# Performance work log

Hardware: AMD Instinct MI355X
Metric: run time of the kernel (lower is better)

The kernel has to match this reference:

```python
import jax, jax.numpy as jnp
import numpy as np

N_NODES = 100000
N_EDGES = 1600000
HIDDEN = 128
STEPS = 4
N_GRAPHS = 64


def setup_inputs() -> dict:
    key = jax.random.key(0)
    ks = jax.random.split(key, 8)
    x = jax.random.normal(ks[0], (N_NODES, HIDDEN), dtype=jnp.float32)
    edge_index = jax.random.randint(ks[1], (2, N_EDGES), 0, N_NODES, dtype=jnp.int64)
    batch = jnp.sort(jax.random.randint(ks[2], (N_NODES,), 0, N_GRAPHS, dtype=jnp.int64))
    s = 1.0 / np.sqrt(HIDDEN)
    weight = jax.random.normal(ks[3], (STEPS, HIDDEN, HIDDEN), dtype=jnp.float32) * s
    w_ih = jax.random.normal(ks[4], (3 * HIDDEN, HIDDEN), dtype=jnp.float32) * s
    w_hh = jax.random.normal(ks[5], (3 * HIDDEN, HIDDEN), dtype=jnp.float32) * s
    b_ih = jnp.zeros((3 * HIDDEN,), dtype=jnp.float32)
    b_hh = jnp.zeros((3 * HIDDEN,), dtype=jnp.float32)
    return {"x": x, "edge_index": edge_index, "batch": batch,
            "weight": weight, "w_ih": w_ih, "w_hh": w_hh,
            "b_ih": b_ih, "b_hh": b_hh}


def _gru_cell(m, h, w_ih, w_hh, b_ih, b_hh):
    # PyTorch GRUCell: gates ordered (r, z, n)
    gi = m @ w_ih.T + b_ih  # [N, 3H]
    gh = h @ w_hh.T + b_hh  # [N, 3H]
    i_r, i_z, i_n = jnp.split(gi, 3, axis=-1)
    h_r, h_z, h_n = jnp.split(gh, 3, axis=-1)
    r = jax.nn.sigmoid(i_r + h_r)
    z = jax.nn.sigmoid(i_z + h_z)
    n = jnp.tanh(i_n + r * h_n)
    return (1.0 - z) * n + z * h


def reference(x, edge_index, batch, weight, w_ih, w_hh, b_ih, b_hh):
    src, dst = edge_index[0], edge_index[1]
    h = x
    for i in range(STEPS):
        m = h @ weight[i]  # [N, H]
        # message = m[src] scattered (add) into dst
        aggr = jax.ops.segment_sum(m[src], dst, num_segments=N_NODES)
        h = _gru_cell(aggr, h, w_ih, w_hh, b_ih, b_hh)
    h = jax.nn.relu(h)
    # global mean pool per graph
    sums = jax.ops.segment_sum(h, batch, num_segments=N_GRAPHS)  # [G, H]
    counts = jax.ops.segment_sum(jnp.ones((N_NODES,), h.dtype), batch, num_segments=N_GRAPHS)
    return sums / jnp.maximum(counts, 1.0)[:, None]
```

## Files before the change

kernel.cpp:

```cpp
#include <hip/hip_runtime.h>

#define N_NODES  100000
#define N_EDGES  1600000
#define HIDDEN   128
#define STEPS    4
#define N_GRAPHS 64
#define NBUCK    256
#define BWID     391
#define BCAP     7168

typedef unsigned short u16;
typedef unsigned int   u32;
typedef unsigned long long u64;
typedef __attribute__((ext_vector_type(8))) short bf16x8;
typedef __attribute__((ext_vector_type(4))) float f32x4;
typedef __attribute__((ext_vector_type(2))) float f32x2;

__device__ inline u16 f2bf(float f) {
  u32 u = __float_as_uint(f);
  u = (u + 0x7FFFu + ((u >> 16) & 1u)) >> 16;
  return (u16)u;
}
__device__ inline float bf2f(u16 b) { return __uint_as_float(((u32)b) << 16); }

__device__ inline float rcp_f(float x) { return __builtin_amdgcn_rcpf(x); }
__device__ inline float sig_f(float x) { return rcp_f(1.f + __expf(-x)); }
__device__ inline float tanh_f(float x) { return 1.f - 2.f * rcp_f(1.f + __expf(2.f * x)); }

__global__ __launch_bounds__(1024) void k_part(const int* __restrict__ esrc,
                                               const int* __restrict__ edst,
                                               int* __restrict__ gcursor,
                                               u32* __restrict__ ebuf) {
  __shared__ int hist[16][NBUCK];
  __shared__ int base[16][NBUCK];
  int tid = threadIdx.x;
  int wv  = tid >> 6;
  #pragma unroll
  for (int i = 0; i < 4; ++i) ((int*)hist)[tid + i * 1024] = 0;
  __syncthreads();
  int e0 = blockIdx.x * 4096;
  int sv[4], dv[4], bk[4], rk[4];
  #pragma unroll
  for (int i = 0; i < 4; ++i) {
    int e = e0 + i * 1024 + tid;
    if (e < N_EDGES) {
      sv[i] = esrc[e];
      dv[i] = edst[e];
      bk[i] = (int)((u32)dv[i] / (u32)BWID);
      rk[i] = atomicAdd(&hist[wv][bk[i]], 1);
    } else bk[i] = -1;
  }
  __syncthreads();
  if (tid < NBUCK) {
    int c[16];
    int sum = 0;
    #pragma unroll
    for (int w = 0; w < 16; ++w) { c[w] = hist[w][tid]; sum += c[w]; }
    int g = atomicAdd(&gcursor[tid], sum);
    #pragma unroll
    for (int w = 0; w < 16; ++w) { base[w][tid] = g; g += c[w]; }
  }
  __syncthreads();
  #pragma unroll
  for (int i = 0; i < 4; ++i) {
    if (bk[i] >= 0) {
      int pos = bk[i] * BCAP + base[wv][bk[i]] + rk[i];
      ebuf[pos] = ((u32)(dv[i] - bk[i] * BWID) << 17) | (u32)sv[i];
    }
  }
}

__global__ void k_bscan(const int* __restrict__ gcursor, int* __restrict__ ebase,
                        float* __restrict__ acc) {
  __shared__ int buf[NBUCK];
  int t = threadIdx.x;
  int v = gcursor[t];
  buf[t] = v;
  __syncthreads();
  for (int off = 1; off < NBUCK; off <<= 1) {
    int u = 0;
    if (t >= off) u = buf[t - off];
    __syncthreads();
    buf[t] += u;
    __syncthreads();
  }
  ebase[t] = buf[t] - v;
  if (t == NBUCK - 1) ebase[NBUCK] = buf[t];
  for (int i = t; i < N_GRAPHS * HIDDEN; i += NBUCK) acc[i] = 0.f;
}

__global__ __launch_bounds__(1024) void k_csr(const u32* __restrict__ ebuf,
                                              const int* __restrict__ ebase,
                                              int* __restrict__ offs,
                                              int* __restrict__ csr) {
  __shared__ int lcnt[512];
  __shared__ int lofs[512];
  int b = blockIdx.x, tid = threadIdx.x;
  int n0 = b * BWID;
  int n1 = min(n0 + BWID, N_NODES);
  int nn = n1 - n0;
  int e0 = ebase[b];
  int cnt = ebase[b + 1] - e0;
  const u32* ebase_p = ebuf + (size_t)b * BCAP;
  if (tid < 512) lcnt[tid] = 0;
  __syncthreads();
  for (int e = tid; e < cnt; e += 1024) {
    int dst = (int)(ebase_p[e] >> 17);
    atomicAdd(&lcnt[dst], 1);
  }
  __syncthreads();
  if (tid < 512) lofs[tid] = lcnt[tid];
  __syncthreads();
  for (int off = 1; off < 512; off <<= 1) {
    int v = 0;
    if (tid < 512 && tid >= off) v = lofs[tid - off];
    __syncthreads();
    if (tid < 512 && tid >= off) lofs[tid] += v;
    __syncthreads();
  }
  int nodeoff = 0;
  if (tid < 512) nodeoff = e0 + lofs[tid] - lcnt[tid];
  if (tid < 512) lofs[tid] = nodeoff;
  if (tid < nn) offs[n0 + tid] = nodeoff;
  if (b == 0 && tid == 0) offs[N_NODES] = N_EDGES;
  __syncthreads();
  for (int e = tid; e < cnt; e += 1024) {
    u32 p = ebase_p[e];
    int src = (int)(p & 0x1FFFFu);
    int dst = (int)(p >> 17);
    int pos = atomicAdd(&lofs[dst], 1);
    csr[pos] = src;
  }
}

__global__ void k_wb(const float* __restrict__ W, const float* __restrict__ w_ih,
                     const float* __restrict__ w_hh, u16* __restrict__ bsw) {
  __shared__ float wrow[128];
  int b = blockIdx.x, st = b >> 8, k = b & 255, t = threadIdx.x;
  if (k < 128) wrow[t] = W[(st * 128 + k) * 128 + t];
  __syncthreads();
  int kc = k >> 5, quad = (k >> 3) & 3, kl = k & 7;
  u16* base = bsw + (size_t)st * 131072 + kc * 16384;
  #pragma unroll
  for (int gq = 0; gq < 4; ++gq) {
    int c = gq * 128 + t;
    float v;
    if (k < 128) {
      if (c < 384) {
        const float* wr = w_ih + c * 128;
        float sacc = 0.f;
        for (int j = 0; j < 128; ++j) sacc += wrow[j] * wr[j];
        v = sacc;
      } else v = 0.f;
    } else {
      int kk = k - 128;
      if (c < 256)      v = w_hh[c * 128 + kk];
      else if (c < 384) v = 0.f;
      else              v = w_hh[(c - 128) * 128 + kk];
    }
    int gi = c >> 7, cw = c & 127;
    int wv = cw >> 5, hu = (cw >> 4) & 1, nl = c & 15;
    int slot = wv * 8 + gi * 2 + hu;
    base[(slot * 4 + quad) * 128 + nl * 8 + kl] = f2bf(v);
  }
}

__global__ void k_convert(const float* __restrict__ x, u16* __restrict__ h0,
                          u16* __restrict__ h1) {
  int i = (blockIdx.x * 256 + threadIdx.x) * 4;
  float4 v = *(const float4*)(x + i);
  u16 o[4] = {f2bf(v.x), f2bf(v.y), f2bf(v.z), f2bf(v.w)};
  *(uint2*)(h0 + i) = *(uint2*)o;
  if (blockIdx.x == 0) {
    int t = threadIdx.x;
    if (t < 64)       ((u32*)(h0 + (size_t)N_NODES * 128))[t] = 0;
    else if (t < 128) ((u32*)(h1 + (size_t)N_NODES * 128))[t - 64] = 0;
  }
}

__device__ inline void acc8(f32x2* a, uint4 p) {
  f32x2 v;
  v.x = __uint_as_float(p.x << 16); v.y = __uint_as_float(p.x & 0xffff0000u);
  a[0] += v;
  v.x = __uint_as_float(p.y << 16); v.y = __uint_as_float(p.y & 0xffff0000u);
  a[1] += v;
  v.x = __uint_as_float(p.z << 16); v.y = __uint_as_float(p.z & 0xffff0000u);
  a[2] += v;
  v.x = __uint_as_float(p.w << 16); v.y = __uint_as_float(p.w & 0xffff0000u);
  a[3] += v;
}
__device__ inline uint4 ldrow(const char* hb, u32 off) {
  return *(const uint4*)(hb + off);
}

__global__ __launch_bounds__(256, 2) void k_fused(
    const u16* __restrict__ h_mat, const int* __restrict__ csr,
    const int* __restrict__ offs, const u16* __restrict__ bsw,
    const float* __restrict__ b_ih, const float* __restrict__ b_hh,
    u16* __restrict__ h_out) {
  __shared__ u16 Asw[8192];

  const int tid  = threadIdx.x;
  const int wave = tid >> 6;
  const int lane = tid & 63;
  const int nl   = lane & 15;
  const int quad = lane >> 4;
  const int row0 = blockIdx.x * 32;

  {
    int snl = tid & 15, squad = (tid >> 4) & 3, sel = tid >> 6;
    if (sel >= 2) {
      int g = sel & 1;
      const u16* row = h_mat + (size_t)(row0 + g * 16 + snl) * 128;
      #pragma unroll
      for (int kc2 = 0; kc2 < 4; ++kc2) {
        uint4 v = *(const uint4*)(row + kc2 * 32 + squad * 8);
        *(uint4*)&Asw[(((g * 8 + 4 + kc2) * 4 + squad) * 16 + snl) * 8] = v;
      }
    }
  }

  {
    const char* hb = (const char*)h_mat;
    const int q   = lane >> 4;
    const int sub = lane & 15;
    const u32 co  = (u32)(sub * 16);
    #pragma unroll 1
    for (int i = 0; i < 8; ++i) {
      int n    = wave * 8 + i;
      int node = row0 + n;
      int beg = offs[node], end = offs[node + 1];
      f32x2 a[4];
      a[0] = a[1] = a[2] = a[3] = (f32x2){0.f, 0.f};
      int j = beg + q;
      for (; j + 12 < end; j += 16) {
        u32 s0 = (u32)csr[j], s1 = (u32)csr[j + 4], s2 = (u32)csr[j + 8], s3 = (u32)csr[j + 12];
        uint4 p0 = ldrow(hb, (s0 << 8) | co);
        uint4 p1 = ldrow(hb, (s1 << 8) | co);
        uint4 p2 = ldrow(hb, (s2 << 8) | co);
        uint4 p3 = ldrow(hb, (s3 << 8) | co);
        acc8(a, p0); acc8(a, p1); acc8(a, p2); acc8(a, p3);
      }
      {
        int j0 = j, j1 = j + 4, j2 = j + 8, j3 = j + 12;
        int t0 = (j0 < end) ? j0 : 0, t1 = (j1 < end) ? j1 : 0;
        int t2 = (j2 < end) ? j2 : 0, t3 = (j3 < end) ? j3 : 0;
        u32 s0 = (u32)csr[t0]; s0 = (j0 < end) ? s0 : (u32)N_NODES;
        u32 s1 = (u32)csr[t1]; s1 = (j1 < end) ? s1 : (u32)N_NODES;
        u32 s2 = (u32)csr[t2]; s2 = (j2 < end) ? s2 : (u32)N_NODES;
        u32 s3 = (u32)csr[t3]; s3 = (j3 < end) ? s3 : (u32)N_NODES;
        uint4 p0 = ldrow(hb, (s0 << 8) | co);
        uint4 p1 = ldrow(hb, (s1 << 8) | co);
        uint4 p2 = ldrow(hb, (s2 << 8) | co);
        uint4 p3 = ldrow(hb, (s3 << 8) | co);
        acc8(a, p0); acc8(a, p1); acc8(a, p2); acc8(a, p3);
      }
      #pragma unroll
      for (int r = 0; r < 4; ++r) {
        a[r].x += __shfl_xor(a[r].x, 16); a[r].x += __shfl_xor(a[r].x, 32);
        a[r].y += __shfl_xor(a[r].y, 16); a[r].y += __shfl_xor(a[r].y, 32);
      }
      if (q == 0) {
        uint4 o;
        o.x = (u32)f2bf(a[0].x) | ((u32)f2bf(a[0].y) << 16);
        o.y = (u32)f2bf(a[1].x) | ((u32)f2bf(a[1].y) << 16);
        o.z = (u32)f2bf(a[2].x) | ((u32)f2bf(a[2].y) << 16);
        o.w = (u32)f2bf(a[3].x) | ((u32)f2bf(a[3].y) << 16);
        int g = n >> 4, snl = n & 15;
        *(uint4*)&Asw[(((g * 8 + (sub >> 2)) * 4 + (sub & 3)) * 16 + snl) * 8] = o;
      }
    }
  }
  __syncthreads();

  const u16* bp = bsw + wave * 8 * 512 + lane * 8;

  f32x4 acc[2][8];
  #pragma unroll
  for (int g = 0; g < 2; ++g)
    #pragma unroll
    for (int u = 0; u < 8; ++u) acc[g][u] = (f32x4){0.f, 0.f, 0.f, 0.f};

  bf16x8 b0[6], b1[6], b2[6];
  #pragma unroll
  for (int i = 0; i < 6; ++i) b0[i] = *(const bf16x8*)(bp + i * 512);
  #pragma unroll
  for (int i = 0; i < 6; ++i) b1[i] = *(const bf16x8*)(bp + 16384 + i * 512);

  #pragma unroll
  for (int kc = 0; kc < 8; ++kc) {
    if (kc < 6) {
      #pragma unroll
      for (int i = 0; i < 6; ++i) {
        int us = (kc + 2 < 4) ? i : (i < 4 ? i : i + 2);
        b2[i] = *(const bf16x8*)(bp + (kc + 2) * 16384 + us * 512);
      }
    }
    bf16x8 a0 = *(const bf16x8*)&Asw[kc * 512 + lane * 8];
    bf16x8 a1 = *(const bf16x8*)&Asw[(8 + kc) * 512 + lane * 8];
    #pragma unroll
    for (int i = 0; i < 6; ++i) {
      int u = (kc < 4) ? i : (i < 4 ? i : i + 2);
      acc[0][u] = __builtin_amdgcn_mfma_f32_16x16x32_bf16(a0, b0[i], acc[0][u], 0, 0, 0);
      acc[1][u] = __builtin_amdgcn_mfma_f32_16x16x32_bf16(a1, b0[i], acc[1][u], 0, 0, 0);
    }
    #pragma unroll
    for (int i = 0; i < 6; ++i) { b0[i] = b1[i]; b1[i] = b2[i]; }
  }

  float bias[8];
  #pragma unroll
  for (int u = 0; u < 8; ++u) {
    int gi = u >> 1, hu = u & 1;
    int cw = wave * 32 + hu * 16 + nl;
    bias[u] = (gi == 0) ? b_ih[cw] + b_hh[cw]
            : (gi == 1) ? b_ih[128 + cw] + b_hh[128 + cw]
            : (gi == 2) ? b_ih[256 + cw]
                        : b_hh[256 + cw];
  }

  #pragma unroll
  for (int g = 0; g < 2; ++g) {
    #pragma unroll
    for (int hu = 0; hu < 2; ++hu) {
      int cw = wave * 32 + hu * 16 + nl;
      int hbase = ((g * 8 + 4 + wave) * 4 + ((hu * 2 + (nl >> 3)) & 3)) * 128 + (nl & 7);
      #pragma unroll
      for (int i = 0; i < 4; ++i) {
        int m = quad * 4 + i;
        float rv = sig_f(acc[g][0 + hu][i] + bias[0 + hu]);
        float zv = sig_f(acc[g][2 + hu][i] + bias[2 + hu]);
        float iv = acc[g][4 + hu][i] + bias[4 + hu];
        float hn = acc[g][6 + hu][i] + bias[6 + hu];
        float hv = bf2f(Asw[hbase + m * 8]);
        float n  = tanh_f(iv + rv * hn);
        float o  = n + zv * (hv - n);
        h_out[(size_t)(row0 + g * 16 + m) * 128 + cw] = f2bf(o);
      }
    }
  }
}

__global__ void k_pool_partial(const u16* __restrict__ h, const int* __restrict__ batch,
                               float* __restrict__ acc) {
  int t = threadIdx.x;
  int node0 = blockIdx.x * 125;
  int node1 = node0 + 125;
  int cur = batch[node0];
  float sum = 0.f;
  for (int r = node0; r < node1; ++r) {
    int g = batch[r];
    if (g != cur) {
      atomicAdd(&acc[cur * 128 + t], sum);
      sum = 0.f;
      cur = g;
    }
    sum += fmaxf(bf2f(h[(size_t)r * 128 + t]), 0.f);
  }
  atomicAdd(&acc[cur * 128 + t], sum);
}

__global__ void k_pool_div(const float* __restrict__ acc, const int* __restrict__ batch,
                           float* __restrict__ out) {
  __shared__ int se[2];
  int g = blockIdx.x, t = threadIdx.x;
  if (t < 2) {
    int target = g + t;
    int lo = 0, hi = N_NODES;
    while (lo < hi) { int mid = (lo + hi) >> 1; if (batch[mid] < target) lo = mid + 1; else hi = mid; }
    se[t] = lo;
  }
  __syncthreads();
  int cnt = se[1] - se[0];
  out[g * 128 + t] = acc[g * 128 + t] / (float)(cnt > 0 ? cnt : 1);
}

extern "C" void kernel_launch(void* const* d_in, const int* in_sizes, int n_in,
                              void* d_out, int out_size, void* d_ws, size_t ws_size,
                              hipStream_t stream) {
  const float* x     = (const float*)d_in[0];
  const int*   edges = (const int*)d_in[1];
  const int*   batch = (const int*)d_in[2];
  const float* W     = (const float*)d_in[3];
  const float* w_ih  = (const float*)d_in[4];
  const float* w_hh  = (const float*)d_in[5];
  const float* b_ih  = (const float*)d_in[6];
  const float* b_hh  = (const float*)d_in[7];
  float* out = (float*)d_out;

  char* w = (char*)d_ws;
  u16* buf0    = (u16*)(w);
  u16* buf1    = (u16*)(w + 25600256);
  u16* bsw     = (u16*)(w + 51200512);
  float* acc   = (float*)(w + 52249088);
  int* offs    = (int*)(w + 52281856);
  int* gcursor = (int*)(w + 52682240);
  int* ebase   = (int*)(w + 52683264);
  int* csr     = (int*)(w + 52684800);
  u32* ebuf    = (u32*)buf1;

  const int* esrc = edges;
  const int* edst = edges + N_EDGES;

  hipMemsetAsync(gcursor, 0, NBUCK * sizeof(int), stream);
  k_part<<<391, 1024, 0, stream>>>(esrc, edst, gcursor, ebuf);
  k_bscan<<<1, NBUCK, 0, stream>>>(gcursor, ebase, acc);
  k_csr<<<NBUCK, 1024, 0, stream>>>(ebuf, ebase, offs, csr);
  k_wb<<<1024, 128, 0, stream>>>(W, w_ih, w_hh, bsw);
  k_convert<<<(N_NODES * HIDDEN) / 1024, 256, 0, stream>>>(x, buf0, buf1);

  u16* hcur = buf0;
  u16* hnxt = buf1;
  for (int st = 0; st < STEPS; ++st) {
    k_fused<<<N_NODES / 32, 256, 0, stream>>>(hcur, csr, offs, bsw + st * 131072,
                                              b_ih, b_hh, hnxt);
    u16* tmp = hcur; hcur = hnxt; hnxt = tmp;
  }
  k_pool_partial<<<800, 128, 0, stream>>>(hcur, batch, acc);
  k_pool_div<<<N_GRAPHS, 128, 0, stream>>>(acc, batch, out);
}
```

Measured before the change: 616.7 us.

## Gather two nodes per wave iteration, swizzle LDS, raise occupancy to three blocks

The neighbor-aggregation loop now processes two destination nodes at once, issuing eight independent row gathers per iteration so more memory latency is in flight. All LDS accesses to the A tile go through an XOR swizzle to reduce bank conflicts, and the h-row staging is spread across all four waves instead of two. Launch bounds raise the target to three blocks per CU, which may force register spills given the large MFMA accumulator and B-fragment state. Pairing nodes also wastes work when the two nodes' degrees differ, because the loop runs to the larger degree.

```diff
diff --git a/kernel.cpp b/kernel.cpp
--- a/kernel.cpp
+++ b/kernel.cpp
@@ -26,6 +26,8 @@
 __device__ inline float rcp_f(float x) { return __builtin_amdgcn_rcpf(x); }
 __device__ inline float sig_f(float x) { return rcp_f(1.f + __expf(-x)); }
 __device__ inline float tanh_f(float x) { return 1.f - 2.f * rcp_f(1.f + __expf(2.f * x)); }
+
+__device__ inline u32 swz(u32 b) { return b ^ (((b >> 8) & 7u) << 4); }
 
 __global__ __launch_bounds__(1024) void k_part(const int* __restrict__ esrc,
                                                const int* __restrict__ edst,
@@ -193,12 +195,13 @@
   return *(const uint4*)(hb + off);
 }
 
-__global__ __launch_bounds__(256, 2) void k_fused(
+__global__ __launch_bounds__(256, 3) void k_fused(
     const u16* __restrict__ h_mat, const int* __restrict__ csr,
     const int* __restrict__ offs, const u16* __restrict__ bsw,
     const float* __restrict__ b_ih, const float* __restrict__ b_hh,
     u16* __restrict__ h_out) {
   __shared__ u16 Asw[8192];
+  char* lds = (char*)Asw;
 
   const int tid  = threadIdx.x;
   const int wave = tid >> 6;
@@ -208,66 +211,77 @@
   const int row0 = blockIdx.x * 32;
 
   {
-    int snl = tid & 15, squad = (tid >> 4) & 3, sel = tid >> 6;
-    if (sel >= 2) {
-      int g = sel & 1;
-      const u16* row = h_mat + (size_t)(row0 + g * 16 + snl) * 128;
-      #pragma unroll
-      for (int kc2 = 0; kc2 < 4; ++kc2) {
-        uint4 v = *(const uint4*)(row + kc2 * 32 + squad * 8);
-        *(uint4*)&Asw[(((g * 8 + 4 + kc2) * 4 + squad) * 16 + snl) * 8] = v;
-      }
+    int snl = tid & 15, squad = (tid >> 4) & 3, w = tid >> 6;
+    int g = w & 1;
+    const u16* row = h_mat + (size_t)(row0 + g * 16 + snl) * 128;
+    #pragma unroll
+    for (int kk = 0; kk < 2; ++kk) {
+      int kc2 = (w >> 1) * 2 + kk;
+      uint4 v = *(const uint4*)(row + kc2 * 32 + squad * 8);
+      u32 b = (u32)(((g * 8 + 4 + kc2) * 4 + squad) * 256 + snl * 16);
+      *(uint4*)(lds + swz(b)) = v;
     }
   }
 
   {
     const char* hb = (const char*)h_mat;
-    const int q   = lane >> 4;
-    const int sub = lane & 15;
-    const u32 co  = (u32)(sub * 16);
+    const int q   = quad;
+    const u32 co  = (u32)(nl * 16);
     #pragma unroll 1
-    for (int i = 0; i < 8; ++i) {
-      int n    = wave * 8 + i;
-      int node = row0 + n;
-      int beg = offs[node], end = offs[node + 1];
-      f32x2 a[4];
-      a[0] = a[1] = a[2] = a[3] = (f32x2){0.f, 0.f};
-      int j = beg + q;
-      for (; j + 12 < end; j += 16) {
-        u32 s0 = (u32)csr[j], s1 = (u32)csr[j + 4], s2 = (u32)csr[j + 8], s3 = (u32)csr[j + 12];
-        uint4 p0 = ldrow(hb, (s0 << 8) | co);
-        uint4 p1 = ldrow(hb, (s1 << 8) | co);
-        uint4 p2 = ldrow(hb, (s2 << 8) | co);
-        uint4 p3 = ldrow(hb, (s3 << 8) | co);
-        acc8(a, p0); acc8(a, p1); acc8(a, p2); acc8(a, p3);
-      }
-      {
-        int j0 = j, j1 = j + 4, j2 = j + 8, j3 = j + 12;
-        int t0 = (j0 < end) ? j0 : 0, t1 = (j1 < end) ? j1 : 0;
-        int t2 = (j2 < end) ? j2 : 0, t3 = (j3 < end) ? j3 : 0;
-        u32 s0 = (u32)csr[t0]; s0 = (j0 < end) ? s0 : (u32)N_NODES;
-        u32 s1 = (u32)csr[t1]; s1 = (j1 < end) ? s1 : (u32)N_NODES;
-        u32 s2 = (u32)csr[t2]; s2 = (j2 < end) ? s2 : (u32)N_NODES;
-        u32 s3 = (u32)csr[t3]; s3 = (j3 < end) ? s3 : (u32)N_NODES;
-        uint4 p0 = ldrow(hb, (s0 << 8) | co);
-        uint4 p1 = ldrow(hb, (s1 << 8) | co);
-        uint4 p2 = ldrow(hb, (s2 << 8) | co);
-        uint4 p3 = ldrow(hb, (s3 << 8) | co);
-        acc8(a, p0); acc8(a, p1); acc8(a, p2); acc8(a, p3);
+    for (int p = 0; p < 4; ++p) {
+      int nA = wave * 8 + p * 2;
+      int node = row0 + nA;
+      int o0 = offs[node], o1 = offs[node + 1], o2 = offs[node + 2];
+      f32x2 aA[4], aB[4];
+      #pragma unroll
+      for (int r = 0; r < 4; ++r) { aA[r] = (f32x2){0.f, 0.f}; aB[r] = (f32x2){0.f, 0.f}; }
+      int jA = o0 + q, jB = o1 + q;
+      int dmax = max(o1 - o0, o2 - o1);
+      int iters = (dmax + 15) >> 4;
+      #pragma unroll 1
+      for (int t = 0; t < iters; ++t) {
+        u32 sa[4], sb[4];
+        #pragma unroll
+        for (int k = 0; k < 4; ++k) {
+          int jj = jA + 4 * k;
+          u32 sv = (u32)csr[jj < o1 ? jj : 0];
+          sa[k] = (jj < o1) ? sv : (u32)N_NODES;
+          jj = jB + 4 * k;
+          sv = (u32)csr[jj < o2 ? jj : 0];
+          sb[k] = (jj < o2) ? sv : (u32)N_NODES;
+        }
+        uint4 pa0 = ldrow(hb, (sa[0] << 8) | co);
+        uint4 pa1 = ldrow(hb, (sa[1] << 8) | co);
+        uint4 pa2 = ldrow(hb, (sa[2] << 8) | co);
+        uint4 pa3 = ldrow(hb, (sa[3] << 8) | co);
+        uint4 pb0 = ldrow(hb, (sb[0] << 8) | co);
+        uint4 pb1 = ldrow(hb, (sb[1] << 8) | co);
+        uint4 pb2 = ldrow(hb, (sb[2] << 8) | co);
+        uint4 pb3 = ldrow(hb, (sb[3] << 8) | co);
+        acc8(aA, pa0); acc8(aA, pa1); acc8(aA, pa2); acc8(aA, pa3);
+        acc8(aB, pb0); acc8(aB, pb1); acc8(aB, pb2); acc8(aB, pb3);
+        jA += 16; jB += 16;
       }
       #pragma unroll
       for (int r = 0; r < 4; ++r) {
-        a[r].x += __shfl_xor(a[r].x, 16); a[r].x += __shfl_xor(a[r].x, 32);
-        a[r].y += __shfl_xor(a[r].y, 16); a[r].y += __shfl_xor(a[r].y, 32);
+        aA[r].x += __shfl_xor(aA[r].x, 16); aA[r].x += __shfl_xor(aA[r].x, 32);
+        aA[r].y += __shfl_xor(aA[r].y, 16); aA[r].y += __shfl_xor(aA[r].y, 32);
+        aB[r].x += __shfl_xor(aB[r].x, 16); aB[r].x += __shfl_xor(aB[r].x, 32);
+        aB[r].y += __shfl_xor(aB[r].y, 16); aB[r].y += __shfl_xor(aB[r].y, 32);
       }
-      if (q == 0) {
+      if (q < 2) {
+        f32x2 w0 = q ? aB[0] : aA[0];
+        f32x2 w1 = q ? aB[1] : aA[1];
+        f32x2 w2 = q ? aB[2] : aA[2];
+        f32x2 w3 = q ? aB[3] : aA[3];
         uint4 o;
-        o.x = (u32)f2bf(a[0].x) | ((u32)f2bf(a[0].y) << 16);
-        o.y = (u32)f2bf(a[1].x) | ((u32)f2bf(a[1].y) << 16);
-        o.z = (u32)f2bf(a[2].x) | ((u32)f2bf(a[2].y) << 16);
-        o.w = (u32)f2bf(a[3].x) | ((u32)f2bf(a[3].y) << 16);
-        int g = n >> 4, snl = n & 15;
-        *(uint4*)&Asw[(((g * 8 + (sub >> 2)) * 4 + (sub & 3)) * 16 + snl) * 8] = o;
+        o.x = (u32)f2bf(w0.x) | ((u32)f2bf(w0.y) << 16);
+        o.y = (u32)f2bf(w1.x) | ((u32)f2bf(w1.y) << 16);
+        o.z = (u32)f2bf(w2.x) | ((u32)f2bf(w2.y) << 16);
+        o.w = (u32)f2bf(w3.x) | ((u32)f2bf(w3.y) << 16);
+        int n = nA + q, g = n >> 4, snl = n & 15;
+        u32 b = (u32)(g * 8192 + nl * 256 + snl * 16);
+        *(uint4*)(lds + swz(b)) = o;
       }
     }
   }
@@ -296,8 +310,8 @@
         b2[i] = *(const bf16x8*)(bp + (kc + 2) * 16384 + us * 512);
       }
     }
-    bf16x8 a0 = *(const bf16x8*)&Asw[kc * 512 + lane * 8];
-    bf16x8 a1 = *(const bf16x8*)&Asw[(8 + kc) * 512 + lane * 8];
+    bf16x8 a0 = *(const bf16x8*)(lds + swz((u32)(kc * 1024 + lane * 16)));
+    bf16x8 a1 = *(const bf16x8*)(lds + swz((u32)((8 + kc) * 1024 + lane * 16)));
     #pragma unroll
     for (int i = 0; i < 6; ++i) {
       int u = (kc < 4) ? i : (i < 4 ? i : i + 2);
@@ -324,7 +338,7 @@
     #pragma unroll
     for (int hu = 0; hu < 2; ++hu) {
       int cw = wave * 32 + hu * 16 + nl;
-      int hbase = ((g * 8 + 4 + wave) * 4 + ((hu * 2 + (nl >> 3)) & 3)) * 128 + (nl & 7);
+      u32 hslot = (u32)((g * 8 + 4 + wave) * 4 + ((hu * 2 + (nl >> 3)) & 3));
       #pragma unroll
       for (int i = 0; i < 4; ++i) {
         int m = quad * 4 + i;
@@ -332,7 +346,8 @@
         float zv = sig_f(acc[g][2 + hu][i] + bias[2 + hu]);
         float iv = acc[g][4 + hu][i] + bias[4 + hu];
         float hn = acc[g][6 + hu][i] + bias[6 + hu];
-        float hv = bf2f(Asw[hbase + m * 8]);
+        u32 hb2 = hslot * 256 + (u32)m * 16 + (u32)(nl & 7) * 2;
+        float hv = bf2f(*(const u16*)(lds + swz(hb2)));
         float n  = tanh_f(iv + rv * hn);
         float o  = n + zv * (hv - n);
         h_out[(size_t)(row0 + g * 16 + m) * 128 + cw] = f2bf(o);
```

Measured after the change: 569.4 us. -7.7%, faster.
